# Performance work log

Hardware: AMD Instinct MI355X
Metric: run time of the kernel (lower is better)

Reference implementation:

```python
import jax, jax.numpy as jnp
import numpy as np
import math

B, S, D, H = 4, 2048, 1024, 16
HD = D // H

def setup_inputs() -> dict:
    key = jax.random.key(0)
    ks = jax.random.split(key, 12)
    sc = 1.0 / math.sqrt(D)
    inp = {
        'q': jax.random.normal(ks[0], (B, S, D), jnp.float32),
        'k': jax.random.normal(ks[1], (B, S, D), jnp.float32),
        'v': jax.random.normal(ks[2], (B, S, D), jnp.float32),
        # causal mask: 1.0 where attention is disallowed (j > i)
        'mask': jnp.broadcast_to(jnp.triu(jnp.ones((S, S), jnp.float32), k=1), (B, S, S)),
        'Wq': jax.random.normal(ks[3], (D, D), jnp.float32) * sc,
        'bq': jnp.zeros((D,), jnp.float32),
        'Wk': jax.random.normal(ks[4], (D, D), jnp.float32) * sc,
        'bk': jnp.zeros((D,), jnp.float32),
        'Wv': jax.random.normal(ks[5], (D, D), jnp.float32) * sc,
        'bv': jnp.zeros((D,), jnp.float32),
        'Wo': jax.random.normal(ks[6], (D, D), jnp.float32) * sc,
        'bo': jnp.zeros((D,), jnp.float32),
    }
    return inp

def reference(q, k, v, mask, Wq, bq, Wk, bk, Wv, bv, Wo, bo):
    # linear projections (torch Linear: x @ W^T + b)
    qp = q @ Wq.T + bq
    kp = k @ Wk.T + bk
    vp = v @ Wv.T + bv
    # split heads: [B,S,D] -> [B,H,S,hd]
    qh = qp.reshape(B, S, H, HD).transpose(0, 2, 1, 3)
    kh = kp.reshape(B, S, H, HD).transpose(0, 2, 1, 3)
    vh = vp.reshape(B, S, H, HD).transpose(0, 2, 1, 3)
    scores = jnp.einsum('bhqd,bhkd->bhqk', qh, kh) / jnp.sqrt(jnp.float32(HD))
    scores = scores + mask[:, None, :, :] * jnp.float32(-100000.0)
    attn = jax.nn.softmax(scores, axis=-1)
    out = jnp.einsum('bhqk,bhkd->bhqd', attn, vh)
    out = out.transpose(0, 2, 1, 3).reshape(B, S, D)
    out = out @ Wo.T + bo
    return (out, kh, vh)
```

## Files before the change

### kernel.cpp

```cpp
#include <hip/hip_runtime.h>
#include <stdint.h>

#define Bn 4
#define Sn 2048
#define Dn 1024
#define Hn 16
#define HDn 64

typedef unsigned short u16;
typedef unsigned int u32;
typedef __attribute__((ext_vector_type(8))) __bf16 bf16x8;
typedef __attribute__((ext_vector_type(4))) float f32x4;
typedef __attribute__((ext_vector_type(16))) float f32x16;
typedef __attribute__((ext_vector_type(4))) u32 u32x4;

#define CEXP 0.18033688011112042f
#define LBIAS 20.0f

#define EXP2F(x) __builtin_amdgcn_exp2f(x)

__device__ __forceinline__ u16 f2bf(float f) {
  union { float f; u32 u; } x; x.f = f;
  u32 r = x.u + 0x7FFFu + ((x.u >> 16) & 1u);
  return (u16)(r >> 16);
}

__device__ __forceinline__ void gload16(const u16* g, u16* l) {
  __builtin_amdgcn_global_load_lds(
      (const __attribute__((address_space(1))) void*)g,
      (__attribute__((address_space(3))) void*)l, 16, 0, 0);
}

__global__ void cvt_all(
    const float* __restrict__ q, const float* __restrict__ k, const float* __restrict__ v,
    const float* __restrict__ wq, const float* __restrict__ wk,
    const float* __restrict__ wv, const float* __restrict__ wo,
    u16* __restrict__ oq, u16* __restrict__ ok, u16* __restrict__ ov,
    u16* __restrict__ owq, u16* __restrict__ owk, u16* __restrict__ owv,
    u16* __restrict__ owo)
{
  const int bid = blockIdx.x;
  const float* in; u16* out; int i;
  if (bid < 24576) {
    const int t3 = bid >> 13;
    in = (t3 == 0) ? q : (t3 == 1) ? k : v;
    out = (t3 == 0) ? oq : (t3 == 1) ? ok : ov;
    i = (bid & 8191) * 256 + threadIdx.x;
  } else {
    const int b2 = bid - 24576, t4 = b2 >> 10;
    in = (t4 == 0) ? wq : (t4 == 1) ? wk : (t4 == 2) ? wv : wo;
    out = (t4 == 0) ? owq : (t4 == 1) ? owk : (t4 == 2) ? owv : owo;
    i = (b2 & 1023) * 256 + threadIdx.x;
  }
  float4 vv = ((const float4*)in)[i];
  ushort4 o;
  o.x = f2bf(vv.x); o.y = f2bf(vv.y); o.z = f2bf(vv.z); o.w = f2bf(vv.w);
  ((ushort4*)out)[i] = o;
}

template<int MODE>
__global__ __launch_bounds__(256, 4) void gemm_bt(
    const u16* __restrict__ A, const u16* __restrict__ W,
    const float* __restrict__ bias,
    float* __restrict__ outF, u16* __restrict__ outB)
{
  __shared__ u16 As[2][2048];
  __shared__ u16 Bs[2][4096];

  const int t = threadIdx.x, w = t >> 6, lane = t & 63;
  int bid = (int)blockIdx.x;
  bid = (bid & 7) * 128 + (bid >> 3);
  const int m0 = (bid >> 3) * 64, n0 = (bid & 7) * 128;
  const int wm = (w & 1) * 32, wn = (w >> 1) * 64;
  const int lrow = lane & 15;

  f32x4 acc[2][4] = {};

  auto stage = [&](int buf, int k0) {
    {
      const int c = t;
      const int row = c >> 2;
      const int off = ((c & 3) ^ (row & 3)) * 8;
      gload16(A + (size_t)(m0 + row) * 1024 + k0 + off, &As[buf][(c & ~63) * 8]);
    }
    #pragma unroll
    for (int i = 0; i < 2; ++i) {
      const int c = i * 256 + t;
      const int row = c >> 2;
      const int off = ((c & 3) ^ (row & 3)) * 8;
      gload16(W + (size_t)(n0 + row) * 1024 + k0 + off, &Bs[buf][(c & ~63) * 8]);
    }
  };

  stage(0, 0);
  for (int kt = 0; kt < 32; ++kt) {
    const int buf = kt & 1;
    __syncthreads();
    if (kt < 31) stage(buf ^ 1, (kt + 1) * 32);
    bf16x8 a[2], b[4];
    #pragma unroll
    for (int i = 0; i < 2; ++i) {
      const int ra = wm + i * 16 + lrow;
      a[i] = *(const bf16x8*)&As[buf][ra * 32 + (((lane >> 4) ^ (ra & 3)) * 8)];
    }
    #pragma unroll
    for (int j = 0; j < 4; ++j) {
      const int rb = wn + j * 16 + lrow;
      b[j] = *(const bf16x8*)&Bs[buf][rb * 32 + (((lane >> 4) ^ (rb & 3)) * 8)];
    }
    #pragma unroll
    for (int i = 0; i < 2; ++i)
      #pragma unroll
      for (int j = 0; j < 4; ++j)
        acc[i][j] = __builtin_amdgcn_mfma_f32_16x16x32_bf16(a[i], b[j], acc[i][j], 0, 0, 0);
  }

  const int g4 = (lane >> 4) * 4;
  #pragma unroll
  for (int i = 0; i < 2; ++i) {
    #pragma unroll
    for (int j = 0; j < 4; ++j) {
      const int gn = n0 + wn + j * 16 + lrow;
      const float bv = bias[gn];
      #pragma unroll
      for (int r = 0; r < 4; ++r) {
        const int gm = m0 + wm + i * 16 + g4 + r;
        const float x = acc[i][j][r] + bv;
        if (MODE == 3) {
          outF[(size_t)gm * 1024 + gn] = x;
        } else {
          const int b_ = gm >> 11, s_ = gm & 2047, h_ = gn >> 6, d_ = gn & 63;
          const size_t hidx = (((size_t)b_ * Hn + h_) * Sn + s_) * HDn + d_;
          if (MODE == 0) outB[hidx] = f2bf(x * CEXP);
          if (MODE == 1) { outF[hidx] = x; outB[hidx] = f2bf(x); }
          if (MODE == 2) { outF[hidx] = x;
                           outB[(((size_t)b_ * Hn + h_) * HDn + d_) * Sn + s_] = f2bf(x); }
        }
      }
    }
  }
}

__global__ __launch_bounds__(256, 4) void attn_kernel(
    const u16* __restrict__ qh, const u16* __restrict__ kh,
    const u16* __restrict__ vt, u16* __restrict__ ao)
{
  __shared__ u16 Ks[2][4096];
  __shared__ u16 Vs[2][4096];

  const int t = threadIdx.x, w = t >> 6, lane = t & 63;
  const int bid = (int)blockIdx.x;
  const int k_ = bid >> 8;
  const int x_ = bid & 7;
  const int c_ = (bid >> 3) & 31;
  const int bh = x_ * 8 + (c_ >> 2);
  const int cq = c_ & 3;
  const int p = (k_ == 0) ? (15 - cq) : (k_ == 1) ? (8 + cq)
              : (k_ == 2) ? (7 - cq) : cq;
  const int l31 = lane & 31, h = lane >> 5;

  const u16* Kb = kh + (size_t)bh * Sn * HDn;
  const u16* Vb = vt + (size_t)bh * HDn * Sn;
  const u16* Qb = qh + (size_t)bh * Sn * HDn;

  const int q0w = p * 128 + w * 32;
  const int qg = q0w + l31;
  const int NT = 2 * p + 2;
  const int NTw = ((q0w + 31) >> 6) + 1;

  bf16x8 qf[4];
  #pragma unroll
  for (int kk = 0; kk < 4; ++kk)
    qf[kk] = *(const bf16x8*)(Qb + (size_t)qg * HDn + kk * 16 + h * 8);

  float l = 0.f;
  f32x16 o0 = {}, o1 = {};

  const int c0 = t, c1 = t + 256;
  const int kr0 = ((c0 >> 8) << 5) + (c0 & 31), kr1 = ((c1 >> 8) << 5) + (c1 & 31);
  const u16* kSrc0 = Kb + (size_t)kr0 * HDn + ((c0 >> 6) & 3) * 16 + ((c0 >> 5) & 1) * 8;
  const u16* kSrc1 = Kb + (size_t)kr1 * HDn + ((c1 >> 6) & 3) * 16 + ((c1 >> 5) & 1) * 8;
  const u16* vSrc0 = Vb + (size_t)kr0 * Sn + (2 * ((c0 >> 6) & 3) + ((c0 >> 5) & 1)) * 8;
  const u16* vSrc1 = Vb + (size_t)kr1 * Sn + (2 * ((c1 >> 6) & 3) + ((c1 >> 5) & 1)) * 8;
  const int d0 = (c0 & ~63) * 8, d1 = (c1 & ~63) * 8;

  auto stage = [&](int buf) {
    gload16(kSrc0, &Ks[buf][d0]);
    gload16(kSrc1, &Ks[buf][d1]);
    gload16(vSrc0, &Vs[buf][d0]);
    gload16(vSrc1, &Vs[buf][d1]);
    kSrc0 += 64 * HDn; kSrc1 += 64 * HDn;
    vSrc0 += 64;       vSrc1 += 64;
  };

  auto unit = [&](int buf, int jt) {
    const u16* Kbuf = &Ks[buf][0];
    const u16* Vbuf = &Vs[buf][0];
    f32x16 s0, s1;
    #pragma unroll
    for (int r = 0; r < 16; ++r) { s0[r] = -LBIAS; s1[r] = -LBIAS; }

    __builtin_amdgcn_s_setprio(1);
    #pragma unroll
    for (int kk = 0; kk < 4; ++kk) {
      bf16x8 k0 = *(const bf16x8*)&Kbuf[(kk * 64 + lane) * 8];
      bf16x8 k1 = *(const bf16x8*)&Kbuf[((4 + kk) * 64 + lane) * 8];
      s0 = __builtin_amdgcn_mfma_f32_32x32x16_bf16(k0, qf[kk], s0, 0, 0, 0);
      s1 = __builtin_amdgcn_mfma_f32_32x32x16_bf16(k1, qf[kk], s1, 0, 0, 0);
    }
    __builtin_amdgcn_s_setprio(0);

    if (jt * 64 + 63 > q0w) {
      const int kvb = jt * 64 + 4 * h;
      #pragma unroll
      for (int r = 0; r < 16; ++r) {
        const int rho = (r & 3) + 8 * (r >> 2);
        s0[r] = (kvb + rho > qg) ? -1e30f : s0[r];
        s1[r] = (kvb + 32 + rho > qg) ? -1e30f : s1[r];
      }
    }

    float sum = 0.f;
    #pragma unroll
    for (int r = 0; r < 16; ++r) { s0[r] = EXP2F(s0[r]); sum += s0[r]; }
    #pragma unroll
    for (int r = 0; r < 16; ++r) { s1[r] = EXP2F(s1[r]); sum += s1[r]; }
    sum += __shfl_xor(sum, 32, 64);
    l += sum;

    u32 w0[8], w1[8];
    #pragma unroll
    for (int i = 0; i < 8; ++i) {
      asm("v_cvt_pk_bf16_f32 %0, %1, %2" : "=v"(w0[i]) : "v"(s0[2 * i]), "v"(s0[2 * i + 1]));
      asm("v_cvt_pk_bf16_f32 %0, %1, %2" : "=v"(w1[i]) : "v"(s1[2 * i]), "v"(s1[2 * i + 1]));
    }
    asm("v_permlane32_swap_b32 %0, %1" : "+v"(w0[0]), "+v"(w0[2]));
    asm("v_permlane32_swap_b32 %0, %1" : "+v"(w0[1]), "+v"(w0[3]));
    asm("v_permlane32_swap_b32 %0, %1" : "+v"(w0[4]), "+v"(w0[6]));
    asm("v_permlane32_swap_b32 %0, %1" : "+v"(w0[5]), "+v"(w0[7]));
    asm("v_permlane32_swap_b32 %0, %1" : "+v"(w1[0]), "+v"(w1[2]));
    asm("v_permlane32_swap_b32 %0, %1" : "+v"(w1[1]), "+v"(w1[3]));
    asm("v_permlane32_swap_b32 %0, %1" : "+v"(w1[4]), "+v"(w1[6]));
    asm("v_permlane32_swap_b32 %0, %1" : "+v"(w1[5]), "+v"(w1[7]));

    __builtin_amdgcn_s_setprio(1);
    #pragma unroll
    for (int s = 0; s < 4; ++s) {
      const u32* wt = (s < 2) ? w0 : w1;
      const int j4 = (s & 1) * 4;
      u32x4 fr = { wt[j4], wt[j4 + 1], wt[j4 + 2], wt[j4 + 3] };
      bf16x8 pf = __builtin_bit_cast(bf16x8, fr);
      bf16x8 v0 = *(const bf16x8*)&Vbuf[(s * 64 + lane) * 8];
      bf16x8 v1 = *(const bf16x8*)&Vbuf[((4 + s) * 64 + lane) * 8];
      o0 = __builtin_amdgcn_mfma_f32_32x32x16_bf16(v0, pf, o0, 0, 0, 0);
      o1 = __builtin_amdgcn_mfma_f32_32x32x16_bf16(v1, pf, o1, 0, 0, 0);
    }
    __builtin_amdgcn_s_setprio(0);
  };

  stage(0);
  for (int jt = 0; jt < NT; ++jt) {
    const int buf = jt & 1;
    __syncthreads();
    if (jt + 1 < NT) stage(buf ^ 1);
    if (jt < NTw) unit(buf, jt);
  }

  const int b_ = bh >> 4, h_ = bh & 15;
  const float rl = 1.0f / l;
  u16* base = ao + ((size_t)b_ * Sn + qg) * Dn + h_ * HDn;
  #pragma unroll
  for (int n = 0; n < 2; ++n)
    #pragma unroll
    for (int u = 0; u < 4; ++u) {
      const f32x16& o = n ? o1 : o0;
      ushort4 ov;
      ov.x = f2bf(o[4 * u + 0] * rl); ov.y = f2bf(o[4 * u + 1] * rl);
      ov.z = f2bf(o[4 * u + 2] * rl); ov.w = f2bf(o[4 * u + 3] * rl);
      *(ushort4*)&base[n * 32 + 8 * u + 4 * h] = ov;
    }
}

extern "C" void kernel_launch(void* const* d_in, const int* in_sizes, int n_in,
                              void* d_out, int out_size, void* d_ws, size_t ws_size,
                              hipStream_t stream)
{
  const float* q  = (const float*)d_in[0];
  const float* k  = (const float*)d_in[1];
  const float* v  = (const float*)d_in[2];
  const float* Wq = (const float*)d_in[4];
  const float* bq = (const float*)d_in[5];
  const float* Wk = (const float*)d_in[6];
  const float* bk = (const float*)d_in[7];
  const float* Wv = (const float*)d_in[8];
  const float* bv = (const float*)d_in[9];
  const float* Wo = (const float*)d_in[10];
  const float* bo = (const float*)d_in[11];

  float* out_o  = (float*)d_out;
  float* out_kh = out_o + (size_t)Bn * Sn * Dn;
  float* out_vh = out_kh + (size_t)Bn * Sn * Dn;

  char* ws = (char*)d_ws;
  const size_t MB = 1ull << 20;
  u16* wq_bf = (u16*)(ws + 0 * MB);
  u16* wk_bf = (u16*)(ws + 2 * MB);
  u16* wv_bf = (u16*)(ws + 4 * MB);
  u16* wo_bf = (u16*)(ws + 6 * MB);
  u16* q_bf  = (u16*)(ws + 8 * MB);
  u16* k_bf  = (u16*)(ws + 24 * MB);
  u16* v_bf  = (u16*)(ws + 40 * MB);
  u16* qh_bf = (u16*)(ws + 56 * MB);
  u16* kh_bf = (u16*)(ws + 72 * MB);
  u16* vt_bf = (u16*)(ws + 88 * MB);
  u16* ao_bf = q_bf;

  cvt_all<<<28672, 256, 0, stream>>>(q, k, v, Wq, Wk, Wv, Wo,
                                     q_bf, k_bf, v_bf,
                                     wq_bf, wk_bf, wv_bf, wo_bf);

  gemm_bt<0><<<1024, 256, 0, stream>>>(q_bf, wq_bf, bq, nullptr, qh_bf);
  gemm_bt<1><<<1024, 256, 0, stream>>>(k_bf, wk_bf, bk, out_kh, kh_bf);
  gemm_bt<2><<<1024, 256, 0, stream>>>(v_bf, wv_bf, bv, out_vh, vt_bf);

  attn_kernel<<<1024, 256, 0, stream>>>(qh_bf, kh_bf, vt_bf, ao_bf);

  gemm_bt<3><<<1024, 256, 0, stream>>>(ao_bf, wo_bf, bo, out_o, nullptr);
}
```

Before: 201.2 us.

## Pair causal query tiles per 2-wave block to balance attention work

The attention kernel now uses 128-thread blocks of two waves. Each block handles two 64-query tiles, tile 31-s and tile s, one after the other, so every block processes the same total number of KV tiles. Previously each block covered 128 queries with four waves, and lower waves sat idle while the block walked KV tiles that only the upper waves needed. The cost is that each K/V tile staged into LDS is shared by only two waves, which raises global-to-LDS traffic per query. It also adds a barrier between the two tiles and changes the launch bounds.

```diff
diff --git a/kernel.cpp b/kernel.cpp
--- a/kernel.cpp
+++ b/kernel.cpp
@@ -141,7 +141,7 @@
   }
 }
 
-__global__ __launch_bounds__(256, 4) void attn_kernel(
+__global__ __launch_bounds__(128, 2) void attn_kernel(
     const u16* __restrict__ qh, const u16* __restrict__ kh,
     const u16* __restrict__ vt, u16* __restrict__ ao)
 {
@@ -150,135 +150,144 @@
 
   const int t = threadIdx.x, w = t >> 6, lane = t & 63;
   const int bid = (int)blockIdx.x;
-  const int k_ = bid >> 8;
   const int x_ = bid & 7;
   const int c_ = (bid >> 3) & 31;
+  const int r_ = bid >> 8;
   const int bh = x_ * 8 + (c_ >> 2);
-  const int cq = c_ & 3;
-  const int p = (k_ == 0) ? (15 - cq) : (k_ == 1) ? (8 + cq)
-              : (k_ == 2) ? (7 - cq) : cq;
+  const int s_ = (c_ & 3) * 4 + r_;
   const int l31 = lane & 31, h = lane >> 5;
 
   const u16* Kb = kh + (size_t)bh * Sn * HDn;
   const u16* Vb = vt + (size_t)bh * HDn * Sn;
   const u16* Qb = qh + (size_t)bh * Sn * HDn;
-
-  const int q0w = p * 128 + w * 32;
-  const int qg = q0w + l31;
-  const int NT = 2 * p + 2;
-  const int NTw = ((q0w + 31) >> 6) + 1;
-
-  bf16x8 qf[4];
+  const int b_ = bh >> 4, h_ = bh & 15;
+
+  int kr[4], kc[4], dd[4];
   #pragma unroll
-  for (int kk = 0; kk < 4; ++kk)
-    qf[kk] = *(const bf16x8*)(Qb + (size_t)qg * HDn + kk * 16 + h * 8);
-
-  float l = 0.f;
-  f32x16 o0 = {}, o1 = {};
-
-  const int c0 = t, c1 = t + 256;
-  const int kr0 = ((c0 >> 8) << 5) + (c0 & 31), kr1 = ((c1 >> 8) << 5) + (c1 & 31);
-  const u16* kSrc0 = Kb + (size_t)kr0 * HDn + ((c0 >> 6) & 3) * 16 + ((c0 >> 5) & 1) * 8;
-  const u16* kSrc1 = Kb + (size_t)kr1 * HDn + ((c1 >> 6) & 3) * 16 + ((c1 >> 5) & 1) * 8;
-  const u16* vSrc0 = Vb + (size_t)kr0 * Sn + (2 * ((c0 >> 6) & 3) + ((c0 >> 5) & 1)) * 8;
-  const u16* vSrc1 = Vb + (size_t)kr1 * Sn + (2 * ((c1 >> 6) & 3) + ((c1 >> 5) & 1)) * 8;
-  const int d0 = (c0 & ~63) * 8, d1 = (c1 & ~63) * 8;
-
-  auto stage = [&](int buf) {
-    gload16(kSrc0, &Ks[buf][d0]);
-    gload16(kSrc1, &Ks[buf][d1]);
-    gload16(vSrc0, &Vs[buf][d0]);
-    gload16(vSrc1, &Vs[buf][d1]);
-    kSrc0 += 64 * HDn; kSrc1 += 64 * HDn;
-    vSrc0 += 64;       vSrc1 += 64;
-  };
-
-  auto unit = [&](int buf, int jt) {
-    const u16* Kbuf = &Ks[buf][0];
-    const u16* Vbuf = &Vs[buf][0];
-    f32x16 s0, s1;
-    #pragma unroll
-    for (int r = 0; r < 16; ++r) { s0[r] = -LBIAS; s1[r] = -LBIAS; }
-
-    __builtin_amdgcn_s_setprio(1);
-    #pragma unroll
-    for (int kk = 0; kk < 4; ++kk) {
-      bf16x8 k0 = *(const bf16x8*)&Kbuf[(kk * 64 + lane) * 8];
-      bf16x8 k1 = *(const bf16x8*)&Kbuf[((4 + kk) * 64 + lane) * 8];
-      s0 = __builtin_amdgcn_mfma_f32_32x32x16_bf16(k0, qf[kk], s0, 0, 0, 0);
-      s1 = __builtin_amdgcn_mfma_f32_32x32x16_bf16(k1, qf[kk], s1, 0, 0, 0);
-    }
-    __builtin_amdgcn_s_setprio(0);
-
-    if (jt * 64 + 63 > q0w) {
-      const int kvb = jt * 64 + 4 * h;
-      #pragma unroll
-      for (int r = 0; r < 16; ++r) {
-        const int rho = (r & 3) + 8 * (r >> 2);
-        s0[r] = (kvb + rho > qg) ? -1e30f : s0[r];
-        s1[r] = (kvb + 32 + rho > qg) ? -1e30f : s1[r];
-      }
-    }
-
-    float sum = 0.f;
-    #pragma unroll
-    for (int r = 0; r < 16; ++r) { s0[r] = EXP2F(s0[r]); sum += s0[r]; }
-    #pragma unroll
-    for (int r = 0; r < 16; ++r) { s1[r] = EXP2F(s1[r]); sum += s1[r]; }
-    sum += __shfl_xor(sum, 32, 64);
-    l += sum;
-
-    u32 w0[8], w1[8];
-    #pragma unroll
-    for (int i = 0; i < 8; ++i) {
-      asm("v_cvt_pk_bf16_f32 %0, %1, %2" : "=v"(w0[i]) : "v"(s0[2 * i]), "v"(s0[2 * i + 1]));
-      asm("v_cvt_pk_bf16_f32 %0, %1, %2" : "=v"(w1[i]) : "v"(s1[2 * i]), "v"(s1[2 * i + 1]));
-    }
-    asm("v_permlane32_swap_b32 %0, %1" : "+v"(w0[0]), "+v"(w0[2]));
-    asm("v_permlane32_swap_b32 %0, %1" : "+v"(w0[1]), "+v"(w0[3]));
-    asm("v_permlane32_swap_b32 %0, %1" : "+v"(w0[4]), "+v"(w0[6]));
-    asm("v_permlane32_swap_b32 %0, %1" : "+v"(w0[5]), "+v"(w0[7]));
-    asm("v_permlane32_swap_b32 %0, %1" : "+v"(w1[0]), "+v"(w1[2]));
-    asm("v_permlane32_swap_b32 %0, %1" : "+v"(w1[1]), "+v"(w1[3]));
-    asm("v_permlane32_swap_b32 %0, %1" : "+v"(w1[4]), "+v"(w1[6]));
-    asm("v_permlane32_swap_b32 %0, %1" : "+v"(w1[5]), "+v"(w1[7]));
-
-    __builtin_amdgcn_s_setprio(1);
-    #pragma unroll
-    for (int s = 0; s < 4; ++s) {
-      const u32* wt = (s < 2) ? w0 : w1;
-      const int j4 = (s & 1) * 4;
-      u32x4 fr = { wt[j4], wt[j4 + 1], wt[j4 + 2], wt[j4 + 3] };
-      bf16x8 pf = __builtin_bit_cast(bf16x8, fr);
-      bf16x8 v0 = *(const bf16x8*)&Vbuf[(s * 64 + lane) * 8];
-      bf16x8 v1 = *(const bf16x8*)&Vbuf[((4 + s) * 64 + lane) * 8];
-      o0 = __builtin_amdgcn_mfma_f32_32x32x16_bf16(v0, pf, o0, 0, 0, 0);
-      o1 = __builtin_amdgcn_mfma_f32_32x32x16_bf16(v1, pf, o1, 0, 0, 0);
-    }
-    __builtin_amdgcn_s_setprio(0);
-  };
-
-  stage(0);
-  for (int jt = 0; jt < NT; ++jt) {
-    const int buf = jt & 1;
+  for (int i = 0; i < 4; ++i) {
+    const int c = t + i * 128;
+    kr[i] = ((c >> 8) << 5) + (c & 31);
+    kc[i] = ((c >> 6) & 3) * 16 + ((c >> 5) & 1) * 8;
+    dd[i] = (c & ~63) * 8;
+  }
+
+  for (int ti = 0; ti < 2; ++ti) {
+    const int tile = ti ? s_ : (31 - s_);
+    const int NT = tile + 1;
+    const int q0w = tile * 64 + w * 32;
+    const int qg = q0w + l31;
+
+    bf16x8 qf[4];
+    #pragma unroll
+    for (int kk = 0; kk < 4; ++kk)
+      qf[kk] = *(const bf16x8*)(Qb + (size_t)qg * HDn + kk * 16 + h * 8);
+
+    float l = 0.f;
+    f32x16 o0 = {}, o1 = {};
+
+    const u16 *kS0 = Kb + (size_t)kr[0] * HDn + kc[0];
+    const u16 *kS1 = Kb + (size_t)kr[1] * HDn + kc[1];
+    const u16 *kS2 = Kb + (size_t)kr[2] * HDn + kc[2];
+    const u16 *kS3 = Kb + (size_t)kr[3] * HDn + kc[3];
+    const u16 *vS0 = Vb + (size_t)kr[0] * Sn + kc[0];
+    const u16 *vS1 = Vb + (size_t)kr[1] * Sn + kc[1];
+    const u16 *vS2 = Vb + (size_t)kr[2] * Sn + kc[2];
+    const u16 *vS3 = Vb + (size_t)kr[3] * Sn + kc[3];
+
+    auto stage = [&](int buf) {
+      gload16(kS0, &Ks[buf][dd[0]]); gload16(kS1, &Ks[buf][dd[1]]);
+      gload16(kS2, &Ks[buf][dd[2]]); gload16(kS3, &Ks[buf][dd[3]]);
+      gload16(vS0, &Vs[buf][dd[0]]); gload16(vS1, &Vs[buf][dd[1]]);
+      gload16(vS2, &Vs[buf][dd[2]]); gload16(vS3, &Vs[buf][dd[3]]);
+      kS0 += 64 * HDn; kS1 += 64 * HDn; kS2 += 64 * HDn; kS3 += 64 * HDn;
+      vS0 += 64; vS1 += 64; vS2 += 64; vS3 += 64;
+    };
+
+    stage(0);
+    for (int jt = 0; jt < NT; ++jt) {
+      const int buf = jt & 1;
+      __syncthreads();
+      if (jt + 1 < NT) stage(buf ^ 1);
+
+      const u16* Kbuf = &Ks[buf][0];
+      const u16* Vbuf = &Vs[buf][0];
+      f32x16 s0, s1;
+      #pragma unroll
+      for (int r = 0; r < 16; ++r) { s0[r] = -LBIAS; s1[r] = -LBIAS; }
+
+      __builtin_amdgcn_s_setprio(1);
+      #pragma unroll
+      for (int kk = 0; kk < 4; ++kk) {
+        bf16x8 k0 = *(const bf16x8*)&Kbuf[(kk * 64 + lane) * 8];
+        bf16x8 k1 = *(const bf16x8*)&Kbuf[((4 + kk) * 64 + lane) * 8];
+        s0 = __builtin_amdgcn_mfma_f32_32x32x16_bf16(k0, qf[kk], s0, 0, 0, 0);
+        s1 = __builtin_amdgcn_mfma_f32_32x32x16_bf16(k1, qf[kk], s1, 0, 0, 0);
+      }
+      __builtin_amdgcn_s_setprio(0);
+
+      if (jt * 64 + 63 > q0w) {
+        const int kvb = jt * 64 + 4 * h;
+        #pragma unroll
+        for (int r = 0; r < 16; ++r) {
+          const int rho = (r & 3) + 8 * (r >> 2);
+          s0[r] = (kvb + rho > qg) ? -1e30f : s0[r];
+          s1[r] = (kvb + 32 + rho > qg) ? -1e30f : s1[r];
+        }
+      }
+
+      float sum = 0.f;
+      #pragma unroll
+      for (int r = 0; r < 16; ++r) { s0[r] = EXP2F(s0[r]); sum += s0[r]; }
+      #pragma unroll
+      for (int r = 0; r < 16; ++r) { s1[r] = EXP2F(s1[r]); sum += s1[r]; }
+      sum += __shfl_xor(sum, 32, 64);
+      l += sum;
+
+      u32 w0[8], w1[8];
+      #pragma unroll
+      for (int i = 0; i < 8; ++i) {
+        asm("v_cvt_pk_bf16_f32 %0, %1, %2" : "=v"(w0[i]) : "v"(s0[2 * i]), "v"(s0[2 * i + 1]));
+        asm("v_cvt_pk_bf16_f32 %0, %1, %2" : "=v"(w1[i]) : "v"(s1[2 * i]), "v"(s1[2 * i + 1]));
+      }
+      asm("v_permlane32_swap_b32 %0, %1" : "+v"(w0[0]), "+v"(w0[2]));
+      asm("v_permlane32_swap_b32 %0, %1" : "+v"(w0[1]), "+v"(w0[3]));
+      asm("v_permlane32_swap_b32 %0, %1" : "+v"(w0[4]), "+v"(w0[6]));
+      asm("v_permlane32_swap_b32 %0, %1" : "+v"(w0[5]), "+v"(w0[7]));
+      asm("v_permlane32_swap_b32 %0, %1" : "+v"(w1[0]), "+v"(w1[2]));
+      asm("v_permlane32_swap_b32 %0, %1" : "+v"(w1[1]), "+v"(w1[3]));
+      asm("v_permlane32_swap_b32 %0, %1" : "+v"(w1[4]), "+v"(w1[6]));
+      asm("v_permlane32_swap_b32 %0, %1" : "+v"(w1[5]), "+v"(w1[7]));
+
+      __builtin_amdgcn_s_setprio(1);
+      #pragma unroll
+      for (int s = 0; s < 4; ++s) {
+        const u32* wt = (s < 2) ? w0 : w1;
+        const int j4 = (s & 1) * 4;
+        u32x4 fr = { wt[j4], wt[j4 + 1], wt[j4 + 2], wt[j4 + 3] };
+        bf16x8 pf = __builtin_bit_cast(bf16x8, fr);
+        bf16x8 v0 = *(const bf16x8*)&Vbuf[(s * 64 + lane) * 8];
+        bf16x8 v1 = *(const bf16x8*)&Vbuf[((4 + s) * 64 + lane) * 8];
+        o0 = __builtin_amdgcn_mfma_f32_32x32x16_bf16(v0, pf, o0, 0, 0, 0);
+        o1 = __builtin_amdgcn_mfma_f32_32x32x16_bf16(v1, pf, o1, 0, 0, 0);
+      }
+      __builtin_amdgcn_s_setprio(0);
+    }
+
+    const float rl = 1.0f / l;
+    u16* base = ao + ((size_t)b_ * Sn + qg) * Dn + h_ * HDn;
+    #pragma unroll
+    for (int n = 0; n < 2; ++n)
+      #pragma unroll
+      for (int u = 0; u < 4; ++u) {
+        const f32x16& o = n ? o1 : o0;
+        ushort4 ov;
+        ov.x = f2bf(o[4 * u + 0] * rl); ov.y = f2bf(o[4 * u + 1] * rl);
+        ov.z = f2bf(o[4 * u + 2] * rl); ov.w = f2bf(o[4 * u + 3] * rl);
+        *(ushort4*)&base[n * 32 + 8 * u + 4 * h] = ov;
+      }
+
     __syncthreads();
-    if (jt + 1 < NT) stage(buf ^ 1);
-    if (jt < NTw) unit(buf, jt);
-  }
-
-  const int b_ = bh >> 4, h_ = bh & 15;
-  const float rl = 1.0f / l;
-  u16* base = ao + ((size_t)b_ * Sn + qg) * Dn + h_ * HDn;
-  #pragma unroll
-  for (int n = 0; n < 2; ++n)
-    #pragma unroll
-    for (int u = 0; u < 4; ++u) {
-      const f32x16& o = n ? o1 : o0;
-      ushort4 ov;
-      ov.x = f2bf(o[4 * u + 0] * rl); ov.y = f2bf(o[4 * u + 1] * rl);
-      ov.z = f2bf(o[4 * u + 2] * rl); ov.w = f2bf(o[4 * u + 3] * rl);
-      *(ushort4*)&base[n * 32 + 8 * u + 4 * h] = ov;
-    }
+  }
 }
 
 extern "C" void kernel_launch(void* const* d_in, const int* in_sizes, int n_in,
@@ -323,7 +332,7 @@
   gemm_bt<1><<<1024, 256, 0, stream>>>(k_bf, wk_bf, bk, out_kh, kh_bf);
   gemm_bt<2><<<1024, 256, 0, stream>>>(v_bf, wv_bf, bv, out_vh, vt_bf);
 
-  attn_kernel<<<1024, 256, 0, stream>>>(qh_bf, kh_bf, vt_bf, ao_bf);
+  attn_kernel<<<1024, 128, 0, stream>>>(qh_bf, kh_bf, vt_bf, ao_bf);
 
   gemm_bt<3><<<1024, 256, 0, stream>>>(ao_bf, wo_bf, bo, out_o, nullptr);
 }
```

After: 214.5 us. +6.6%, slower.
